# Kernel tuning notes

Measured on AMD Instinct MI355X. Metric: run time of the kernel, lower is better.

Reference implementation:

```python
import jax, jax.numpy as jnp
import numpy as np

N = 50000   # nodes
R = 3       # relations
E = 300000  # edges per relation
H, D = 4, 32  # heads, per-head dim (hidden_feat=128)
IN, HID, OUT = 128, 128, 64
SLOPE = 0.2  # DGL GATConv leaky_relu negative slope


def setup_inputs() -> dict:
    key = jax.random.key(0)
    ks = jax.random.split(key, 12)
    s = 0.05
    return {
        "x": jax.random.normal(ks[0], (N, IN), jnp.float32),
        "edges": jax.random.randint(ks[1], (R, 2, E), 0, N, jnp.int64),
        "W1": jax.random.normal(ks[2], (R, IN, H * D), jnp.float32) * s,
        "al1": jax.random.normal(ks[3], (R, H, D), jnp.float32) * s,
        "ar1": jax.random.normal(ks[4], (R, H, D), jnp.float32) * s,
        "b1": jnp.zeros((R, H, D), jnp.float32),
        "W2": jax.random.normal(ks[5], (R, HID, H * D), jnp.float32) * s,
        "al2": jax.random.normal(ks[6], (R, H, D), jnp.float32) * s,
        "ar2": jax.random.normal(ks[7], (R, H, D), jnp.float32) * s,
        "b2": jnp.zeros((R, H, D), jnp.float32),
        "Wl": jax.random.normal(ks[8], (HID, OUT), jnp.float32) * s,
        "bl": jnp.zeros((OUT,), jnp.float32),
    }


def rgat_layer(h, edges, W, al, ar, b):
    """HeteroGraphConv(sum) of per-relation GATConv. h: [N,F]. Returns [N,H,D]."""
    out = jnp.zeros((N, H, D), h.dtype)
    for r in range(R):  # small fixed relation count
        src, dst = edges[r, 0], edges[r, 1]
        feat = (h @ W[r]).reshape(N, H, D)                  # per-relation projection
        el = jnp.einsum("nhd,hd->nh", feat, al[r])          # [N,H]
        er = jnp.einsum("nhd,hd->nh", feat, ar[r])          # [N,H]
        e = jax.nn.leaky_relu(el[src] + er[dst], SLOPE)      # [E,H]
        # edge softmax over incoming edges per destination node
        emax = jax.ops.segment_max(e, dst, num_segments=N)   # [N,H]
        ex = jnp.exp(e - emax[dst])
        denom = jax.ops.segment_sum(ex, dst, num_segments=N) # [N,H]
        alpha = ex / denom[dst]                               # [E,H]
        msg = feat[src] * alpha[:, :, None]                   # [E,H,D]
        out = out + jax.ops.segment_sum(msg, dst, num_segments=N) + b[r]
    return out


def reference(x, edges, W1, al1, ar1, b1, W2, al2, ar2, b2, Wl, bl):
    h = rgat_layer(x, edges, W1, al1, ar1, b1).reshape(N, H * D)
    h = jax.nn.relu(h)  # dropout is identity in eval mode
    h = rgat_layer(h, edges, W2, al2, ar2, b2).reshape(N, H * D)
    return h @ Wl + bl  # [N, OUT]
```

## Files before the change

### kernel.cpp

```cpp
#include <hip/hip_runtime.h>
#include <hip/hip_bf16.h>
#include <hip/hip_fp16.h>
#include <type_traits>

#define Nn 50000
#define RR 3
#define EE 300000

typedef __attribute__((ext_vector_type(8))) short short8;
typedef __attribute__((ext_vector_type(4))) short short4v;
typedef __attribute__((ext_vector_type(4))) float floatx4;

__device__ __forceinline__ short f2bf(float f) {
    __hip_bfloat16 h = __float2bfloat16(f);
    return *reinterpret_cast<short*>(&h);
}


__global__ void count_wswz_kernel(const int* __restrict__ edges, int* __restrict__ counts,
                                  int* __restrict__ ord,
                                  const float* __restrict__ W1, const float* __restrict__ W2,
                                  const float* __restrict__ Wl, short* __restrict__ Z) {
    int bx = blockIdx.x;
    if (bx >= 488) {
        int idx = (bx - 488) * 256 + threadIdx.x;
        if (idx >= 1024) return;
        int lane = idx & 63;
        int nt = (idx >> 6) & 3;
        int kt = idx >> 8;
        int n = nt * 16 + (lane & 15);
        int k0 = kt * 32 + (lane >> 4) * 8;
        short8 v;
        #pragma unroll
        for (int j = 0; j < 8; ++j) v[j] = f2bf(Wl[(size_t)(k0 + j) * 64 + n]);
        *(short8*)&Z[98304 + (size_t)idx * 8] = v;
        return;
    }
    if (bx >= 440) {
        int idx = (bx - 440) * 256 + threadIdx.x;
        if (idx >= 12288) return;
        int lane = idx & 63;
        int nt = (idx >> 6) & 7;
        int kt = (idx >> 9) & 3;
        int rl = idx >> 11;
        int layer = rl / 3, r = rl % 3;
        const float* W = (layer ? W2 : W1) + (size_t)r * 16384;
        int n = nt * 16 + (lane & 15);
        int k0 = kt * 32 + (lane >> 4) * 8;
        short8 v;
        #pragma unroll
        for (int j = 0; j < 8; ++j) v[j] = f2bf(W[(size_t)(k0 + j) * 128 + n]);
        *(short8*)&Z[(size_t)idx * 8] = v;
        return;
    }
    int i = bx * 256 + threadIdx.x;
    if (i >= RR * EE / 8) return;
    int g = i * 8;
    int r = g / EE, e0 = g - r * EE;
    const int* db = &edges[(size_t)r * 2 * EE + EE + e0];
    int4 d0 = *(const int4*)db;
    int4 d1 = *(const int4*)(db + 4);
    int* cb = counts + r * Nn;
    int4 o0, o1;
    o0.x = atomicAdd(&cb[d0.x], 1);
    o0.y = atomicAdd(&cb[d0.y], 1);
    o0.z = atomicAdd(&cb[d0.z], 1);
    o0.w = atomicAdd(&cb[d0.w], 1);
    o1.x = atomicAdd(&cb[d1.x], 1);
    o1.y = atomicAdd(&cb[d1.y], 1);
    o1.z = atomicAdd(&cb[d1.z], 1);
    o1.w = atomicAdd(&cb[d1.w], 1);
    *(int4*)&ord[g] = o0;
    *(int4*)&ord[g + 4] = o1;
}

__global__ __launch_bounds__(256) void alloc_kernel(const int* __restrict__ counts,
                                                    int* __restrict__ row_start,
                                                    int* __restrict__ totals) {
    __shared__ int s[256];
    __shared__ int base_s;
    int r = blockIdx.y;
    int tid = threadIdx.x;
    int n = blockIdx.x * 256 + tid;
    int idx = r * Nn + n;
    int c = (n < Nn) ? counts[idx] : 0;
    s[tid] = c;
    __syncthreads();
    #pragma unroll
    for (int off = 1; off < 256; off <<= 1) {
        int v = 0;
        if (tid >= off) v = s[tid - off];
        __syncthreads();
        if (tid >= off) s[tid] += v;
        __syncthreads();
    }
    if (tid == 255) base_s = atomicAdd(&totals[r], s[255]);
    __syncthreads();
    if (n < Nn) row_start[idx] = base_s + s[tid] - c;
}

__global__ void scatter_kernel(const int* __restrict__ edges, const int* __restrict__ ord,
                               const int* __restrict__ row_start, int* __restrict__ csr_s) {
    int i = blockIdx.x * blockDim.x + threadIdx.x;
    if (i >= RR * EE / 8) return;
    int g = i * 8;
    int r = g / EE, e0 = g - r * EE;
    const int* sb = &edges[(size_t)r * 2 * EE + e0];
    const int* db = sb + EE;
    int4 s0 = *(const int4*)sb, s1 = *(const int4*)(sb + 4);
    int4 d0 = *(const int4*)db, d1 = *(const int4*)(db + 4);
    int4 o0 = *(const int4*)&ord[g], o1 = *(const int4*)&ord[g + 4];
    const int* rs = row_start + r * Nn;
    int* cs = csr_s + (size_t)r * EE;
    cs[rs[d0.x] + o0.x] = s0.x;
    cs[rs[d0.y] + o0.y] = s0.y;
    cs[rs[d0.z] + o0.z] = s0.z;
    cs[rs[d0.w] + o0.w] = s0.w;
    cs[rs[d1.x] + o1.x] = s1.x;
    cs[rs[d1.y] + o1.y] = s1.y;
    cs[rs[d1.z] + o1.z] = s1.z;
    cs[rs[d1.w] + o1.w] = s1.w;
}


template<typename TA>
__global__ __launch_bounds__(256) void gemm_proj_mfma(const TA* __restrict__ A,
                                                      const short* __restrict__ Z,
                                                      const float* __restrict__ al,
                                                      const float* __restrict__ ar,
                                                      __half* __restrict__ C,
                                                      float* __restrict__ el,
                                                      float* __restrict__ er) {
    __shared__ short A_lds[64 * 136];
    __shared__ float al_lds[384], ar_lds[384];
    int tid = threadIdx.x;
    int row0 = blockIdx.x * 64;
    if (tid < 128) { al_lds[256 + tid] = al[256 + tid]; ar_lds[256 + tid] = ar[256 + tid]; }
    al_lds[tid] = al[tid]; ar_lds[tid] = ar[tid];
    if constexpr (std::is_same<TA, float>::value) {
        #pragma unroll
        for (int p = 0; p < 8; ++p) {
            int f = p * 256 + tid;
            int row = f >> 5;
            int c4 = (f & 31) * 4;
            float4 v = make_float4(0.f, 0.f, 0.f, 0.f);
            if (row0 + row < Nn) v = *(const float4*)&A[(size_t)(row0 + row) * 128 + c4];
            short4v sv;
            sv[0] = f2bf(v.x); sv[1] = f2bf(v.y); sv[2] = f2bf(v.z); sv[3] = f2bf(v.w);
            *(short4v*)&A_lds[row * 136 + c4] = sv;
        }
    } else {
        #pragma unroll
        for (int p = 0; p < 4; ++p) {
            int c = p * 256 + tid;
            int row = c >> 4, c8 = (c & 15) * 8;
            short8 v = (short8)(0);
            if (row0 + row < Nn) v = *(const short8*)&A[(size_t)(row0 + row) * 128 + c8];
            *(short8*)&A_lds[row * 136 + c8] = v;
        }
    }
    __syncthreads();
    int wave = tid >> 6, lane = tid & 63;
    int m = lane & 15, q = lane >> 4;
    short8 af[4];
    #pragma unroll
    for (int kt = 0; kt < 4; ++kt)
        af[kt] = *(short8*)&A_lds[(wave * 16 + m) * 136 + kt * 32 + q * 8];
    __syncthreads();
    __half* lds_h = (__half*)A_lds;
    int row8 = tid >> 2;
    int hh = tid & 3;
    for (int r = 0; r < RR; ++r) {
        floatx4 acc[8];
        #pragma unroll
        for (int nt = 0; nt < 8; ++nt) acc[nt] = (floatx4)(0.f);
        const short* Zr = Z + (size_t)r * 16384;
        #pragma unroll
        for (int kt = 0; kt < 4; ++kt) {
            #pragma unroll
            for (int nt = 0; nt < 8; ++nt) {
                short8 bf = *(const short8*)&Zr[(size_t)(kt * 8 + nt) * 512 + lane * 8];
                acc[nt] = __builtin_amdgcn_mfma_f32_16x16x32_bf16(af[kt], bf, acc[nt], 0, 0, 0);
            }
        }
        #pragma unroll
        for (int nt = 0; nt < 8; ++nt) {
            int col = nt * 16 + m;
            #pragma unroll
            for (int reg = 0; reg < 4; ++reg)
                lds_h[(wave * 16 + q * 4 + reg) * 136 + col] = __float2half(acc[nt][reg]);
        }
        __syncthreads();
        __half* Cr = C + (size_t)r * Nn * 128;
        #pragma unroll
        for (int p = 0; p < 4; ++p) {
            int lin = p * 256 + tid;
            int row = lin >> 4, c8 = (lin & 15) * 8;
            if (row0 + row < Nn)
                *(short8*)&Cr[(size_t)(row0 + row) * 128 + c8] = *(short8*)&lds_h[row * 136 + c8];
        }
        {
            const __half2* fp = (const __half2*)&lds_h[row8 * 136 + hh * 32];
            const float* alp = &al_lds[r * 128 + hh * 32];
            const float* arp = &ar_lds[r * 128 + hh * 32];
            float sl = 0.f, sr = 0.f;
            #pragma unroll
            for (int d = 0; d < 16; ++d) {
                float2 v = __half22float2(fp[d]);
                sl += v.x * alp[2 * d] + v.y * alp[2 * d + 1];
                sr += v.x * arp[2 * d] + v.y * arp[2 * d + 1];
            }
            if (row0 + row8 < Nn) {
                size_t ei = (size_t)(r * Nn + row0 + row8) * 4 + hh;
                el[ei] = sl;
                er[ei] = sr;
            }
        }
        __syncthreads();
    }
}


__global__ __launch_bounds__(256) void final_mfma(const short* __restrict__ A,
                                                  const short* __restrict__ Zl,
                                                  const float* __restrict__ bl,
                                                  float* __restrict__ out) {
    __shared__ __align__(16) short A_lds[64 * 136];
    int tid = threadIdx.x;
    int row0 = blockIdx.x * 64;
    #pragma unroll
    for (int p = 0; p < 4; ++p) {
        int c = p * 256 + tid;
        int row = c >> 4, c8 = (c & 15) * 8;
        short8 v = (short8)(0);
        if (row0 + row < Nn) v = *(const short8*)&A[(size_t)(row0 + row) * 128 + c8];
        *(short8*)&A_lds[row * 136 + c8] = v;
    }
    __syncthreads();
    int wave = tid >> 6, lane = tid & 63;
    int m = lane & 15, q = lane >> 4;
    short8 af[4];
    #pragma unroll
    for (int kt = 0; kt < 4; ++kt)
        af[kt] = *(short8*)&A_lds[(wave * 16 + m) * 136 + kt * 32 + q * 8];
    __syncthreads();
    float* lds_f = (float*)A_lds;
    floatx4 acc[4];
    #pragma unroll
    for (int nt = 0; nt < 4; ++nt) acc[nt] = (floatx4)(0.f);
    #pragma unroll
    for (int kt = 0; kt < 4; ++kt) {
        #pragma unroll
        for (int nt = 0; nt < 4; ++nt) {
            short8 bf = *(const short8*)&Zl[(size_t)(kt * 4 + nt) * 512 + lane * 8];
            acc[nt] = __builtin_amdgcn_mfma_f32_16x16x32_bf16(af[kt], bf, acc[nt], 0, 0, 0);
        }
    }
    #pragma unroll
    for (int nt = 0; nt < 4; ++nt) {
        int col = nt * 16 + m;
        #pragma unroll
        for (int reg = 0; reg < 4; ++reg)
            lds_f[(wave * 16 + q * 4 + reg) * 68 + col] = acc[nt][reg];
    }
    __syncthreads();
    #pragma unroll
    for (int p = 0; p < 4; ++p) {
        int lin = p * 256 + tid;
        int row = lin >> 4, c4 = (lin & 15) * 4;
        if (row0 + row < Nn) {
            float4 bias = *(const float4*)&bl[c4];
            float4 v = *(float4*)&lds_f[row * 68 + c4];
            v.x += bias.x; v.y += bias.y; v.z += bias.z; v.w += bias.w;
            *(float4*)&out[(size_t)(row0 + row) * 64 + c4] = v;
        }
    }
}


template<int OUT_MODE>
__global__ __launch_bounds__(256) void agg_kernel(const __half2* __restrict__ feat2,
                                                  const float* __restrict__ el,
                                                  const float* __restrict__ er,
                                                  const int* __restrict__ csr_s,
                                                  const int* __restrict__ row_start,
                                                  const int* __restrict__ counts,
                                                  const float* __restrict__ b,
                                                  short* __restrict__ out) {
    int wave = threadIdx.x >> 6;
    int lane = threadIdx.x & 63;
    int n = blockIdx.x * 4 + wave;
    if (n >= Nn) return;
    int h = lane >> 4;
    int hl = lane & 15;
    int grp = lane & 48;
    int t2 = lane * 2;
    int cntA[RR], stA[RR], sC[RR];
    #pragma unroll
    for (int r = 0; r < RR; ++r) {
        cntA[r] = counts[r * Nn + n];
        stA[r] = row_start[r * Nn + n];
    }
    #pragma unroll
    for (int r = 0; r < RR; ++r) {
        sC[r] = 0;
        if (hl < cntA[r]) sC[r] = csr_s[(size_t)r * EE + stA[r] + hl];
    }
    float erv[RR];
    #pragma unroll
    for (int r = 0; r < RR; ++r) erv[r] = er[(size_t)(r * Nn + n) * 4 + h];
    unsigned pC[RR];
    #pragma unroll
    for (int r = 0; r < RR; ++r) {
        float x = el[(size_t)(r * Nn + sC[r]) * 4 + h] + erv[r];
        x = (x > 0.f) ? x : 0.2f * x;
        unsigned wb = (hl < cntA[r]) ? (unsigned)__half_as_ushort(__float2half(__expf(x))) : 0u;
        pC[r] = (unsigned)sC[r] | (wb << 16);
    }
    float accx = b[t2] + b[128 + t2] + b[256 + t2];
    float accy = b[t2 + 1] + b[128 + t2 + 1] + b[256 + t2 + 1];
    #pragma unroll
    for (int r = 0; r < RR; ++r) {
        int cnt = cntA[r];
        if (cnt == 0) continue;
        const __half2* fr = feat2 + (size_t)r * Nn * 64;
        float den = 0.f, numx = 0.f, numy = 0.f;
        unsigned p_l = pC[r];
        int i0 = 0;
        while (true) {
            int mm = cnt - i0; if (mm > 16) mm = 16;
            int mm8 = (mm + 7) & ~7;
            for (int j = 0; j < mm8; j += 8) {
                unsigned u0 = __shfl(p_l, grp | j);
                unsigned u1 = __shfl(p_l, grp | (j + 1));
                unsigned u2 = __shfl(p_l, grp | (j + 2));
                unsigned u3 = __shfl(p_l, grp | (j + 3));
                unsigned u4 = __shfl(p_l, grp | (j + 4));
                unsigned u5 = __shfl(p_l, grp | (j + 5));
                unsigned u6 = __shfl(p_l, grp | (j + 6));
                unsigned u7 = __shfl(p_l, grp | (j + 7));
                __half2 f0 = fr[(size_t)(u0 & 0xFFFFu) * 64 + lane];
                __half2 f1 = fr[(size_t)(u1 & 0xFFFFu) * 64 + lane];
                __half2 f2 = fr[(size_t)(u2 & 0xFFFFu) * 64 + lane];
                __half2 f3 = fr[(size_t)(u3 & 0xFFFFu) * 64 + lane];
                __half2 f4 = fr[(size_t)(u4 & 0xFFFFu) * 64 + lane];
                __half2 f5 = fr[(size_t)(u5 & 0xFFFFu) * 64 + lane];
                __half2 f6 = fr[(size_t)(u6 & 0xFFFFu) * 64 + lane];
                __half2 f7 = fr[(size_t)(u7 & 0xFFFFu) * 64 + lane];
                float w0 = __half2float(__ushort_as_half((unsigned short)(u0 >> 16)));
                float w1 = __half2float(__ushort_as_half((unsigned short)(u1 >> 16)));
                float w2 = __half2float(__ushort_as_half((unsigned short)(u2 >> 16)));
                float w3 = __half2float(__ushort_as_half((unsigned short)(u3 >> 16)));
                float w4 = __half2float(__ushort_as_half((unsigned short)(u4 >> 16)));
                float w5 = __half2float(__ushort_as_half((unsigned short)(u5 >> 16)));
                float w6 = __half2float(__ushort_as_half((unsigned short)(u6 >> 16)));
                float w7 = __half2float(__ushort_as_half((unsigned short)(u7 >> 16)));
                float2 g0 = __half22float2(f0), g1 = __half22float2(f1);
                float2 g2 = __half22float2(f2), g3 = __half22float2(f3);
                float2 g4 = __half22float2(f4), g5 = __half22float2(f5);
                float2 g6 = __half22float2(f6), g7 = __half22float2(f7);
                den += ((w0 + w1) + (w2 + w3)) + ((w4 + w5) + (w6 + w7));
                numx += (w0 * g0.x + w1 * g1.x + w2 * g2.x + w3 * g3.x)
                      + (w4 * g4.x + w5 * g5.x + w6 * g6.x + w7 * g7.x);
                numy += (w0 * g0.y + w1 * g1.y + w2 * g2.y + w3 * g3.y)
                      + (w4 * g4.y + w5 * g5.y + w6 * g6.y + w7 * g7.y);
            }
            i0 += 16;
            if (i0 >= cnt) break;
            int s_t = 0;
            if (i0 + hl < cnt) s_t = csr_s[(size_t)r * EE + stA[r] + i0 + hl];
            float x = el[(size_t)(r * Nn + s_t) * 4 + h] + erv[r];
            x = (x > 0.f) ? x : 0.2f * x;
            unsigned wb = (i0 + hl < cnt) ? (unsigned)__half_as_ushort(__float2half(__expf(x))) : 0u;
            p_l = (unsigned)s_t | (wb << 16);
        }
        float inv = 1.f / den;
        accx += numx * inv;
        accy += numy * inv;
    }
    short2 pk;
    if constexpr (OUT_MODE == 1) {
        pk.x = f2bf(fmaxf(accx, 0.f));
        pk.y = f2bf(fmaxf(accy, 0.f));
    } else {
        pk.x = f2bf(accx);
        pk.y = f2bf(accy);
    }
    *(short2*)&out[(size_t)n * 128 + t2] = pk;
}


extern "C" void kernel_launch(void* const* d_in, const int* in_sizes, int n_in,
                              void* d_out, int out_size, void* d_ws, size_t ws_size,
                              hipStream_t stream) {
    const float* x   = (const float*)d_in[0];
    const int*  edges = (const int*)d_in[1];
    const float* W1  = (const float*)d_in[2];
    const float* al1 = (const float*)d_in[3];
    const float* ar1 = (const float*)d_in[4];
    const float* b1  = (const float*)d_in[5];
    const float* W2  = (const float*)d_in[6];
    const float* al2 = (const float*)d_in[7];
    const float* ar2 = (const float*)d_in[8];
    const float* b2  = (const float*)d_in[9];
    const float* Wl  = (const float*)d_in[10];
    const float* bl  = (const float*)d_in[11];
    float* out = (float*)d_out;

    __half* feat  = (__half*)d_ws;
    short* Z      = (short*)(feat + (size_t)RR * Nn * 128);
    float* el     = (float*)(Z + 106496);
    float* er     = el + (size_t)RR * Nn * 4;
    short* outb16 = (short*)(er + (size_t)RR * Nn * 4);
    int* counts    = (int*)(outb16 + (size_t)Nn * 128);
    int* totals    = counts + RR * Nn;
    int* row_start = totals + 4;
    int* ord       = row_start + RR * Nn;
    int* csr_s     = ord + RR * EE;

    const int rowBlocks  = (Nn + 63) / 64;
    const int nodeBlocks = (Nn + 255) / 256;
    const int aggBlocks  = (Nn + 3) / 4;
    const int edge8Blocks = (RR * EE / 8 + 255) / 256;

    hipMemsetAsync(counts, 0, (size_t)(RR * Nn + 4) * sizeof(int), stream);
    count_wswz_kernel<<<492, 256, 0, stream>>>(edges, counts, ord, W1, W2, Wl, Z);
    alloc_kernel<<<dim3(nodeBlocks, RR), 256, 0, stream>>>(counts, row_start, totals);
    scatter_kernel<<<edge8Blocks, 256, 0, stream>>>(edges, ord, row_start, csr_s);

    gemm_proj_mfma<float><<<rowBlocks, 256, 0, stream>>>(x, Z, al1, ar1, feat, el, er);
    agg_kernel<1><<<aggBlocks, 256, 0, stream>>>((const __half2*)feat, el, er, csr_s, row_start, counts, b1, outb16);

    gemm_proj_mfma<short><<<rowBlocks, 256, 0, stream>>>(outb16, Z + 49152, al2, ar2, feat, el, er);
    agg_kernel<2><<<aggBlocks, 256, 0, stream>>>((const __half2*)feat, el, er, csr_s, row_start, counts, b2, outb16);

    final_mfma<<<rowBlocks, 256, 0, stream>>>(outb16, Z + 98304, bl, out);
}
```

Before: 307.9 us.

## Fuse final linear layer into second aggregation kernel epilogue

Removes the separate final_mfma kernel by having the layer-2 aggregation block stage its 4 node rows in shared memory and run the 128x64 bf16 MFMA projection plus bias directly, writing the fp32 output. This avoids writing and re-reading the bf16 hidden buffer and one kernel launch. The cost is a block-wide barrier, MFMA tiles that are three-quarters zero padding (16 rows computed for 4 nodes), and one wave doing the epilogue while the others idle.

```diff
diff --git a/kernel.cpp b/kernel.cpp
--- a/kernel.cpp
+++ b/kernel.cpp
@@ -221,63 +221,6 @@
 }
 
 
-__global__ __launch_bounds__(256) void final_mfma(const short* __restrict__ A,
-                                                  const short* __restrict__ Zl,
-                                                  const float* __restrict__ bl,
-                                                  float* __restrict__ out) {
-    __shared__ __align__(16) short A_lds[64 * 136];
-    int tid = threadIdx.x;
-    int row0 = blockIdx.x * 64;
-    #pragma unroll
-    for (int p = 0; p < 4; ++p) {
-        int c = p * 256 + tid;
-        int row = c >> 4, c8 = (c & 15) * 8;
-        short8 v = (short8)(0);
-        if (row0 + row < Nn) v = *(const short8*)&A[(size_t)(row0 + row) * 128 + c8];
-        *(short8*)&A_lds[row * 136 + c8] = v;
-    }
-    __syncthreads();
-    int wave = tid >> 6, lane = tid & 63;
-    int m = lane & 15, q = lane >> 4;
-    short8 af[4];
-    #pragma unroll
-    for (int kt = 0; kt < 4; ++kt)
-        af[kt] = *(short8*)&A_lds[(wave * 16 + m) * 136 + kt * 32 + q * 8];
-    __syncthreads();
-    float* lds_f = (float*)A_lds;
-    floatx4 acc[4];
-    #pragma unroll
-    for (int nt = 0; nt < 4; ++nt) acc[nt] = (floatx4)(0.f);
-    #pragma unroll
-    for (int kt = 0; kt < 4; ++kt) {
-        #pragma unroll
-        for (int nt = 0; nt < 4; ++nt) {
-            short8 bf = *(const short8*)&Zl[(size_t)(kt * 4 + nt) * 512 + lane * 8];
-            acc[nt] = __builtin_amdgcn_mfma_f32_16x16x32_bf16(af[kt], bf, acc[nt], 0, 0, 0);
-        }
-    }
-    #pragma unroll
-    for (int nt = 0; nt < 4; ++nt) {
-        int col = nt * 16 + m;
-        #pragma unroll
-        for (int reg = 0; reg < 4; ++reg)
-            lds_f[(wave * 16 + q * 4 + reg) * 68 + col] = acc[nt][reg];
-    }
-    __syncthreads();
-    #pragma unroll
-    for (int p = 0; p < 4; ++p) {
-        int lin = p * 256 + tid;
-        int row = lin >> 4, c4 = (lin & 15) * 4;
-        if (row0 + row < Nn) {
-            float4 bias = *(const float4*)&bl[c4];
-            float4 v = *(float4*)&lds_f[row * 68 + c4];
-            v.x += bias.x; v.y += bias.y; v.z += bias.z; v.w += bias.w;
-            *(float4*)&out[(size_t)(row0 + row) * 64 + c4] = v;
-        }
-    }
-}
-
-
 template<int OUT_MODE>
 __global__ __launch_bounds__(256) void agg_kernel(const __half2* __restrict__ feat2,
                                                   const float* __restrict__ el,
@@ -286,11 +229,19 @@
                                                   const int* __restrict__ row_start,
                                                   const int* __restrict__ counts,
                                                   const float* __restrict__ b,
-                                                  short* __restrict__ out) {
+                                                  short* __restrict__ out,
+                                                  const short* __restrict__ Zl,
+                                                  const float* __restrict__ bl,
+                                                  float* __restrict__ fout) {
+    __shared__ __align__(16) short h_lds[16 * 128];
     int wave = threadIdx.x >> 6;
     int lane = threadIdx.x & 63;
     int n = blockIdx.x * 4 + wave;
-    if (n >= Nn) return;
+    if constexpr (OUT_MODE == 2) {
+        for (int i = 512 + threadIdx.x; i < 2048; i += 256) h_lds[i] = 0;
+    } else {
+        if (n >= Nn) return;
+    }
     int h = lane >> 4;
     int hl = lane & 15;
     int grp = lane & 48;
@@ -378,15 +329,47 @@
         accx += numx * inv;
         accy += numy * inv;
     }
-    short2 pk;
     if constexpr (OUT_MODE == 1) {
+        short2 pk;
         pk.x = f2bf(fmaxf(accx, 0.f));
         pk.y = f2bf(fmaxf(accy, 0.f));
+        *(short2*)&out[(size_t)n * 128 + t2] = pk;
     } else {
+        short2 pk;
         pk.x = f2bf(accx);
         pk.y = f2bf(accy);
-    }
-    *(short2*)&out[(size_t)n * 128 + t2] = pk;
+        *(short2*)&h_lds[wave * 128 + t2] = pk;
+        __syncthreads();
+        if (threadIdx.x < 64) {
+            int m = lane & 15, q = lane >> 4;
+            short8 af[4];
+            #pragma unroll
+            for (int kt = 0; kt < 4; ++kt)
+                af[kt] = *(short8*)&h_lds[m * 128 + kt * 32 + q * 8];
+            floatx4 acc4[4];
+            #pragma unroll
+            for (int nt = 0; nt < 4; ++nt) acc4[nt] = (floatx4)(0.f);
+            #pragma unroll
+            for (int kt = 0; kt < 4; ++kt) {
+                #pragma unroll
+                for (int nt = 0; nt < 4; ++nt) {
+                    short8 bf = *(const short8*)&Zl[(size_t)(kt * 4 + nt) * 512 + lane * 8];
+                    acc4[nt] = __builtin_amdgcn_mfma_f32_16x16x32_bf16(af[kt], bf, acc4[nt], 0, 0, 0);
+                }
+            }
+            if (q == 0) {
+                int n0 = blockIdx.x * 4;
+                #pragma unroll
+                for (int nt = 0; nt < 4; ++nt) {
+                    int col = nt * 16 + m;
+                    float bv = bl[col];
+                    #pragma unroll
+                    for (int reg = 0; reg < 4; ++reg)
+                        fout[(size_t)(n0 + reg) * 64 + col] = acc4[nt][reg] + bv;
+                }
+            }
+        }
+    }
 }
 
 
@@ -420,7 +403,7 @@
 
     const int rowBlocks  = (Nn + 63) / 64;
     const int nodeBlocks = (Nn + 255) / 256;
-    const int aggBlocks  = (Nn + 3) / 4;
+    const int aggBlocks  = Nn / 4;
     const int edge8Blocks = (RR * EE / 8 + 255) / 256;
 
     hipMemsetAsync(counts, 0, (size_t)(RR * Nn + 4) * sizeof(int), stream);
@@ -429,10 +412,10 @@
     scatter_kernel<<<edge8Blocks, 256, 0, stream>>>(edges, ord, row_start, csr_s);
 
     gemm_proj_mfma<float><<<rowBlocks, 256, 0, stream>>>(x, Z, al1, ar1, feat, el, er);
-    agg_kernel<1><<<aggBlocks, 256, 0, stream>>>((const __half2*)feat, el, er, csr_s, row_start, counts, b1, outb16);
+    agg_kernel<1><<<aggBlocks, 256, 0, stream>>>((const __half2*)feat, el, er, csr_s, row_start,
+                                                 counts, b1, outb16, nullptr, nullptr, nullptr);
 
     gemm_proj_mfma<short><<<rowBlocks, 256, 0, stream>>>(outb16, Z + 49152, al2, ar2, feat, el, er);
-    agg_kernel<2><<<aggBlocks, 256, 0, stream>>>((const __half2*)feat, el, er, csr_s, row_start, counts, b2, outb16);
-
-    final_mfma<<<rowBlocks, 256, 0, stream>>>(outb16, Z + 98304, bl, out);
-}
+    agg_kernel<2><<<aggBlocks, 256, 0, stream>>>((const __half2*)feat, el, er, csr_s, row_start,
+                                                 counts, b2, nullptr, Z + 98304, bl, out);
+}
```

New measurement: 319.6 us. 3.8% more time.
